# Performance work log

Measured on AMD Instinct MI355X. Metric: run time of the kernel, lower is better.

## Reference

```python
import jax, jax.numpy as jnp
import numpy as np

B, CH, H, W, D = 2, 32, 256, 512, 192


def setup_inputs() -> dict:
    key = jax.random.key(0)
    ks = jax.random.split(key, 10)
    def w(k, shape, fan_in):
        return jax.random.normal(k, shape, jnp.float32) * (1.0 / np.sqrt(fan_in))
    return {
        "x": jax.random.normal(ks[0], (B, CH, H, W), jnp.float32),
        "y": jax.random.normal(ks[1], (B, CH, H, W), jnp.float32),
        # encoder: 1x1 convs ch->64->32->1 (shared for x and y)
        "w1": w(ks[2], (64, CH), CH), "b1": w(ks[3], (64,), CH),
        "w2": w(ks[4], (32, 64), 64), "b2": w(ks[5], (32,), 64),
        "w3": w(ks[6], (1, 32), 32), "b3": w(ks[7], (1,), 32),
        # decoderl: 1x1 conv maxdisp->maxdisp (original code applies decoderl to BOTH volumes)
        "wd": w(ks[8], (D, D), D), "bd": w(ks[9], (D,), D),
    }


def _conv1x1(w, b, h):  # [O,C] x [B,C,H,W] -> [B,O,H,W]
    return jnp.einsum("oc,bchw->bohw", w, h) + b[None, :, None, None]


def _encoder(x, w1, b1, w2, b2, w3, b3):
    h = jax.nn.relu(x)
    h = jax.nn.relu(_conv1x1(w1, b1, h))
    h = jax.nn.relu(_conv1x1(w2, b2, h))
    h = jax.nn.relu(_conv1x1(w3, b3, h))
    return h[:, 0]  # squeeze channel -> [B,H,W]


def _cost_volumes(xf, yf):
    # costx[b,d,h,w] = xf[b,h,w+d] * yf[b,h,w]   (0 where w+d >= W)
    # costy[b,d,h,w] = xf[b,h,w]   * yf[b,h,w-d] (0 where w-d < 0)
    dgrid = jnp.arange(D)
    wgrid = jnp.arange(W)
    x_pad = jnp.pad(xf, ((0, 0), (0, 0), (0, D)))          # zero pad right
    xg = x_pad[:, :, wgrid[None, :] + dgrid[:, None]]       # [B,H,D,W]
    costx = (xg * yf[:, :, None, :]).transpose(0, 2, 1, 3)  # [B,D,H,W]
    y_pad = jnp.pad(yf, ((0, 0), (0, 0), (D, 0)))           # zero pad left
    yg = y_pad[:, :, wgrid[None, :] - dgrid[:, None] + D]   # [B,H,D,W]
    costy = (xf[:, :, None, :] * yg).transpose(0, 2, 1, 3)  # [B,D,H,W]
    return costx, costy


def reference(x, y, w1, b1, w2, b2, w3, b3, wd, bd):
    xf = _encoder(x, w1, b1, w2, b2, w3, b3)
    yf = _encoder(y, w1, b1, w2, b2, w3, b3)
    costx, costy = _cost_volumes(xf, yf)
    probx = jax.nn.softmax(_conv1x1(wd, bd, costx), axis=1)
    proby = jax.nn.softmax(_conv1x1(wd, bd, costy), axis=1)  # decoderl used for both, as in source
    disp_vals = jnp.arange(D, dtype=probx.dtype)
    dispx = jnp.einsum("bdhw,d->bhw", probx, disp_vals)
    dispy = jnp.einsum("bdhw,d->bhw", proby, disp_vals)
    return dispx, dispy
```

## Files before the change

kernel.cpp:

```cpp
#include <hip/hip_runtime.h>


typedef __attribute__((ext_vector_type(8)))  __bf16 bf16x8;
typedef __attribute__((ext_vector_type(4)))  float  f32x4;
typedef __attribute__((ext_vector_type(16))) float  f32x16;

#define MFMA32(a,b,c) __builtin_amdgcn_mfma_f32_32x32x16_bf16((a),(b),(c),0,0,0)
#define MFMA16(a,b,c) __builtin_amdgcn_mfma_f32_16x16x32_bf16((a),(b),(c),0,0,0)

constexpr int WW  = 512;
constexpr int HW  = 256 * 512;
constexpr int CHW = 32 * HW;
constexpr float LOG2E = 1.4426950408889634f;

constexpr size_t XFB_OFF = 0;
constexpr int    STB     = 25600;
constexpr size_t WDP_OFF = 2 * 262144 * 2;
constexpr size_t BDP_OFF = WDP_OFF + 3 * STB;

__global__ __launch_bounds__(512)
void panet_encode(const float* __restrict__ gx,  const float* __restrict__ gy,
                  const float* __restrict__ gw1, const float* __restrict__ gb1,
                  const float* __restrict__ gw2, const float* __restrict__ gb2,
                  const float* __restrict__ gw3, const float* __restrict__ gb3,
                  const float* __restrict__ gwd, const float* __restrict__ gbd,
                  char* __restrict__ ws)
{
  const int blk = blockIdx.x;
  const int tid = threadIdx.x;

  if (blk >= 1024) {
    const int pi = blk - 1024;
    unsigned short* wdp = (unsigned short*)(ws + WDP_OFF);
    for (int idx = tid; idx < 12 * 200; idx += 512) {
      const int oo = idx / 200;
      const int k  = idx - oo * 200;
      const int o  = 12 * pi + oo;
      unsigned short v = 0;
      if (k < 192) v = __builtin_bit_cast(unsigned short, (__bf16)gwd[o * 192 + k]);
      wdp[(o >> 6) * 12800 + (o & 63) * 200 + k] = v;
    }
    if (pi == 0) {
      float* bdp = (float*)(ws + BDP_OFF);
      if (tid < 192) bdp[tid] = gbd[tid] * LOG2E;
    }
    return;
  }

  const int t    = blk >> 9;
  const int bh   = blk & 511;
  const int lane = tid & 63;
  const int m    = lane & 15;
  const int g    = lane >> 4;
  const int wid  = tid >> 6;

  bf16x8 A1[4], A2[2][2];
  f32x4  bias1[4], bias2[2], w3v[2];
  #pragma unroll
  for (int Mt = 0; Mt < 4; ++Mt) {
    const float* p = gw1 + (16 * Mt + m) * 32 + 4 * g;
    const f32x4 u0 = *(const f32x4*)p;
    const f32x4 u1 = *(const f32x4*)(p + 16);
    #pragma unroll
    for (int j = 0; j < 4; ++j) { A1[Mt][j] = (__bf16)u0[j]; A1[Mt][j + 4] = (__bf16)u1[j]; }
    bias1[Mt] = *(const f32x4*)(gb1 + 16 * Mt + 4 * g);
  }
  #pragma unroll
  for (int Mt = 0; Mt < 2; ++Mt) {
    #pragma unroll
    for (int s = 0; s < 2; ++s) {
      const float* p = gw2 + (16 * Mt + m) * 64 + 32 * s + 4 * g;
      const f32x4 u0 = *(const f32x4*)p;
      const f32x4 u1 = *(const f32x4*)(p + 16);
      #pragma unroll
      for (int j = 0; j < 4; ++j) { A2[Mt][s][j] = (__bf16)u0[j]; A2[Mt][s][j + 4] = (__bf16)u1[j]; }
    }
    bias2[Mt] = *(const f32x4*)(gb2 + 16 * Mt + 4 * g);
    w3v[Mt]   = *(const f32x4*)(gw3 + 16 * Mt + 4 * g);
  }
  const float b3s = gb3[0];
  const f32x4 zf4 = {0.f, 0.f, 0.f, 0.f};
  const float* base = (t ? gy : gx) + (bh >> 8) * CHW + (bh & 255) * WW;
  unsigned short* xfb = (unsigned short*)(ws + XFB_OFF) + t * 262144 + bh * 512;

  for (int u = wid; u < 32; u += 8) {
    const int w0 = u << 4;
    const float* src = base + w0 + m;

    bf16x8 B1;
    #pragma unroll
    for (int j = 0; j < 8; ++j) {
      const int c = 16 * (j >> 2) + 4 * g + (j & 3);
      B1[j] = (__bf16)fmaxf(src[c * HW], 0.f);
    }
    f32x4 acc1[4];
    #pragma unroll
    for (int Mt = 0; Mt < 4; ++Mt) acc1[Mt] = MFMA16(A1[Mt], B1, zf4);

    bf16x8 B2[2];
    #pragma unroll
    for (int s = 0; s < 2; ++s) {
      #pragma unroll
      for (int j = 0; j < 4; ++j) {
        B2[s][j]     = (__bf16)fmaxf(acc1[2 * s][j]     + bias1[2 * s][j],     0.f);
        B2[s][j + 4] = (__bf16)fmaxf(acc1[2 * s + 1][j] + bias1[2 * s + 1][j], 0.f);
      }
    }
    f32x4 acc2[2];
    #pragma unroll
    for (int Mt = 0; Mt < 2; ++Mt)
      acc2[Mt] = MFMA16(A2[Mt][1], B2[1], MFMA16(A2[Mt][0], B2[0], zf4));

    float s3 = 0.f;
    #pragma unroll
    for (int Mt = 0; Mt < 2; ++Mt)
      #pragma unroll
      for (int r = 0; r < 4; ++r)
        s3 += w3v[Mt][r] * fmaxf(acc2[Mt][r] + bias2[Mt][r], 0.f);
    s3 += __shfl_xor(s3, 16);
    s3 += __shfl_xor(s3, 32);
    const float val = fmaxf(s3 + b3s, 0.f);

    if (lane < 16)
      xfb[w0 + m] = __builtin_bit_cast(unsigned short, (__bf16)val);
  }
}

constexpr int CPS    = 1424;
constexpr int K2_HK  = 76800;
constexpr int K2_BD  = K2_HK + 8 * CPS;
constexpr int K2_LDS = K2_BD + 768;

__global__ __launch_bounds__(512)
void panet_corr(const char* __restrict__ ws, float* __restrict__ gout)
{
  __shared__ __align__(16) char lds[K2_LDS];
  const int blk  = blockIdx.x;
  const int dir  = blk >> 9;
  const int bh   = blk & 511;
  const int tid  = threadIdx.x;
  const int lane = tid & 63;
  const int l31  = lane & 31;
  const int h    = lane >> 5;
  const int wid  = tid >> 6;

  const unsigned short* xfbu = (const unsigned short*)(ws + XFB_OFF);
  const unsigned short* hs = xfbu + (dir ? 262144 : 0) + bh * 512;
  const unsigned short* ss = xfbu + (dir ? 0 : 262144) + bh * 512;

  {
    const f32x4* src = (const f32x4*)(ws + WDP_OFF);
    f32x4* dst = (f32x4*)lds;
    #pragma unroll 5
    for (int i = tid; i < 4800; i += 512) dst[i] = src[i];
    if (tid < 192)
      ((float*)(lds + K2_BD))[tid] = ((const float*)(ws + BDP_OFF))[tid];
  }
  for (int e = tid; e < 712; e += 512) {
    #pragma unroll
    for (int c = 0; c < 8; ++c) {
      const int j = e + c;
      unsigned short v = 0;
      if (j <= 511) v = hs[dir ? (511 - j) : j];
      ((unsigned short*)(lds + K2_HK + c * CPS))[e] = v;
    }
  }
  __syncthreads();

  const char* bptr[2]; float sc[2];
  #pragma unroll
  for (int ct = 0; ct < 2; ++ct) {
    const int col = wid * 64 + ct * 32 + l31;
    const int I0  = dir ? (511 - col) : col;
    const int cc  = I0 & 7;
    bptr[ct] = lds + K2_HK + cc * CPS + 2 * (I0 - cc) + 16 * h;
    sc[ct]  = LOG2E * __builtin_bit_cast(float, (unsigned)ss[col] << 16);
  }

  float stS0 = 0.f, stS1 = 0.f, stW0 = 0.f, stW1 = 0.f;

  for (int s = 0; s < 3; ++s) {
    const char* abase = lds + (64 * s + l31) * 400 + 16 * h;
    f32x16 a00 = {0}, a01 = {0}, a10 = {0}, a11 = {0};
    #pragma unroll 4
    for (int ks = 0; ks < 12; ++ks) {
      const bf16x8 af0 = *(const bf16x8*)(abase + 32 * ks);
      const bf16x8 af1 = *(const bf16x8*)(abase + 12800 + 32 * ks);
      const bf16x8 bf0 = *(const bf16x8*)(bptr[0] + 32 * ks);
      const bf16x8 bf1 = *(const bf16x8*)(bptr[1] + 32 * ks);
      a00 = MFMA32(af0, bf0, a00);
      a01 = MFMA32(af0, bf1, a01);
      a10 = MFMA32(af1, bf0, a10);
      a11 = MFMA32(af1, bf1, a11);
    }

    f32x4 bdr0[4], bdr1[4];
    #pragma unroll
    for (int q = 0; q < 4; ++q) {
      bdr0[q] = *(const f32x4*)(lds + K2_BD + (64 * s + 8 * q + 4 * h) * 4);
      bdr1[q] = *(const f32x4*)(lds + K2_BD + (64 * s + 8 * q + 4 * h + 32) * 4);
    }
    const float obase = (float)(64 * s + 4 * h);

    #pragma unroll
    for (int ct = 0; ct < 2; ++ct) {
      float ls0 = 0.f, ls1 = 0.f, lw0 = 0.f, lw1 = 0.f;
      #pragma unroll
      for (int q = 0; q < 4; ++q) {
        #pragma unroll
        for (int r = 0; r < 4; ++r) {
          const int i = 4 * q + r;
          const float L0 = fmaf(sc[ct], (ct ? a01 : a00)[i], bdr0[q][r]);
          const float L1 = fmaf(sc[ct], (ct ? a11 : a10)[i], bdr1[q][r]);
          const float p0 = __builtin_amdgcn_exp2f(L0);
          const float p1 = __builtin_amdgcn_exp2f(L1);
          const float c  = (float)(r + 8 * q);
          ls0 += p0;  ls1 += p1;
          lw0 = fmaf(c, p0, lw0);
          lw1 = fmaf(c + 32.f, p1, lw1);
        }
      }
      const float ls = ls0 + ls1;
      const float lw = fmaf(obase, ls, lw0 + lw1);
      if (ct == 0) { stS0 += ls; stW0 += lw; }
      else         { stS1 += ls; stW1 += lw; }
    }
  }

  float* outp = gout + dir * 262144 + bh * 512;
  #pragma unroll
  for (int ct = 0; ct < 2; ++ct) {
    float sr = ct ? stS1 : stS0;
    float wr = ct ? stW1 : stW0;
    sr += __shfl_xor(sr, 32);
    wr += __shfl_xor(wr, 32);
    if (lane < 32) outp[wid * 64 + ct * 32 + l31] = wr / sr;
  }
}

extern "C" void kernel_launch(void* const* d_in, const int* in_sizes, int n_in,
                              void* d_out, int out_size, void* d_ws, size_t ws_size,
                              hipStream_t stream) {
  const float* x  = (const float*)d_in[0];
  const float* y  = (const float*)d_in[1];
  const float* w1 = (const float*)d_in[2];
  const float* b1 = (const float*)d_in[3];
  const float* w2 = (const float*)d_in[4];
  const float* b2 = (const float*)d_in[5];
  const float* w3 = (const float*)d_in[6];
  const float* b3 = (const float*)d_in[7];
  const float* wd = (const float*)d_in[8];
  const float* bd = (const float*)d_in[9];
  char* ws = (char*)d_ws;

  panet_encode<<<1040, 512, 0, stream>>>(x, y, w1, b1, w2, b2, w3, b3, wd, bd, ws);
  panet_corr<<<1024, 512, 0, stream>>>(ws, (float*)d_out);
}
```

Baseline: 81.36 us.

## Halve corr block size and give each wave four column tiles

The correlation kernel now runs 256 threads per block, and each wave computes 128 output columns (four 32-wide tiles) instead of 64. Each A-fragment load from LDS is reused across four MFMAs instead of two, which cuts LDS traffic per MFMA and halves the per-block weight-staging cost per wave. In exchange each wave holds twice as many accumulators (8 f32x16 tiles), which raises register pressure and may lower occupancy. With fewer waves per block, each wave also does more of the LDS fill.

```diff
diff --git a/kernel.cpp b/kernel.cpp
--- a/kernel.cpp
+++ b/kernel.cpp
@@ -131,7 +131,7 @@
 constexpr int K2_BD  = K2_HK + 8 * CPS;
 constexpr int K2_LDS = K2_BD + 768;
 
-__global__ __launch_bounds__(512)
+__global__ __launch_bounds__(256)
 void panet_corr(const char* __restrict__ ws, float* __restrict__ gout)
 {
   __shared__ __align__(16) char lds[K2_LDS];
@@ -151,12 +151,12 @@
   {
     const f32x4* src = (const f32x4*)(ws + WDP_OFF);
     f32x4* dst = (f32x4*)lds;
-    #pragma unroll 5
-    for (int i = tid; i < 4800; i += 512) dst[i] = src[i];
+    #pragma unroll 4
+    for (int i = tid; i < 4800; i += 256) dst[i] = src[i];
     if (tid < 192)
       ((float*)(lds + K2_BD))[tid] = ((const float*)(ws + BDP_OFF))[tid];
   }
-  for (int e = tid; e < 712; e += 512) {
+  for (int e = tid; e < 712; e += 256) {
     #pragma unroll
     for (int c = 0; c < 8; ++c) {
       const int j = e + c;
@@ -167,51 +167,51 @@
   }
   __syncthreads();
 
-  const char* bptr[2]; float sc[2];
-  #pragma unroll
-  for (int ct = 0; ct < 2; ++ct) {
-    const int col = wid * 64 + ct * 32 + l31;
+  int boff[4]; float sc[4];
+  #pragma unroll
+  for (int ct = 0; ct < 4; ++ct) {
+    const int col = wid * 128 + ct * 32 + l31;
     const int I0  = dir ? (511 - col) : col;
     const int cc  = I0 & 7;
-    bptr[ct] = lds + K2_HK + cc * CPS + 2 * (I0 - cc) + 16 * h;
+    boff[ct] = K2_HK + cc * CPS + 2 * (I0 - cc) + 16 * h;
     sc[ct]  = LOG2E * __builtin_bit_cast(float, (unsigned)ss[col] << 16);
   }
 
-  float stS0 = 0.f, stS1 = 0.f, stW0 = 0.f, stW1 = 0.f;
+  float stS[4] = {0.f, 0.f, 0.f, 0.f};
+  float stW[4] = {0.f, 0.f, 0.f, 0.f};
 
   for (int s = 0; s < 3; ++s) {
     const char* abase = lds + (64 * s + l31) * 400 + 16 * h;
-    f32x16 a00 = {0}, a01 = {0}, a10 = {0}, a11 = {0};
-    #pragma unroll 4
+    f32x16 a0[4] = {{0}, {0}, {0}, {0}};
+    f32x16 a1[4] = {{0}, {0}, {0}, {0}};
+    #pragma unroll 2
     for (int ks = 0; ks < 12; ++ks) {
       const bf16x8 af0 = *(const bf16x8*)(abase + 32 * ks);
       const bf16x8 af1 = *(const bf16x8*)(abase + 12800 + 32 * ks);
-      const bf16x8 bf0 = *(const bf16x8*)(bptr[0] + 32 * ks);
-      const bf16x8 bf1 = *(const bf16x8*)(bptr[1] + 32 * ks);
-      a00 = MFMA32(af0, bf0, a00);
-      a01 = MFMA32(af0, bf1, a01);
-      a10 = MFMA32(af1, bf0, a10);
-      a11 = MFMA32(af1, bf1, a11);
-    }
-
-    f32x4 bdr0[4], bdr1[4];
-    #pragma unroll
-    for (int q = 0; q < 4; ++q) {
-      bdr0[q] = *(const f32x4*)(lds + K2_BD + (64 * s + 8 * q + 4 * h) * 4);
-      bdr1[q] = *(const f32x4*)(lds + K2_BD + (64 * s + 8 * q + 4 * h + 32) * 4);
-    }
+      bf16x8 bf[4];
+      #pragma unroll
+      for (int ct = 0; ct < 4; ++ct)
+        bf[ct] = *(const bf16x8*)(lds + boff[ct] + 32 * ks);
+      #pragma unroll
+      for (int ct = 0; ct < 4; ++ct) {
+        a0[ct] = MFMA32(af0, bf[ct], a0[ct]);
+        a1[ct] = MFMA32(af1, bf[ct], a1[ct]);
+      }
+    }
+
     const float obase = (float)(64 * s + 4 * h);
-
-    #pragma unroll
-    for (int ct = 0; ct < 2; ++ct) {
+    #pragma unroll
+    for (int ct = 0; ct < 4; ++ct) {
       float ls0 = 0.f, ls1 = 0.f, lw0 = 0.f, lw1 = 0.f;
       #pragma unroll
       for (int q = 0; q < 4; ++q) {
+        const f32x4 bd0 = *(const f32x4*)(lds + K2_BD + (64 * s + 8 * q + 4 * h) * 4);
+        const f32x4 bd1 = *(const f32x4*)(lds + K2_BD + (64 * s + 8 * q + 4 * h + 32) * 4);
         #pragma unroll
         for (int r = 0; r < 4; ++r) {
           const int i = 4 * q + r;
-          const float L0 = fmaf(sc[ct], (ct ? a01 : a00)[i], bdr0[q][r]);
-          const float L1 = fmaf(sc[ct], (ct ? a11 : a10)[i], bdr1[q][r]);
+          const float L0 = fmaf(sc[ct], a0[ct][i], bd0[r]);
+          const float L1 = fmaf(sc[ct], a1[ct][i], bd1[r]);
           const float p0 = __builtin_amdgcn_exp2f(L0);
           const float p1 = __builtin_amdgcn_exp2f(L1);
           const float c  = (float)(r + 8 * q);
@@ -222,19 +222,19 @@
       }
       const float ls = ls0 + ls1;
       const float lw = fmaf(obase, ls, lw0 + lw1);
-      if (ct == 0) { stS0 += ls; stW0 += lw; }
-      else         { stS1 += ls; stW1 += lw; }
+      stS[ct] += ls;
+      stW[ct] += lw;
     }
   }
 
   float* outp = gout + dir * 262144 + bh * 512;
   #pragma unroll
-  for (int ct = 0; ct < 2; ++ct) {
-    float sr = ct ? stS1 : stS0;
-    float wr = ct ? stW1 : stW0;
+  for (int ct = 0; ct < 4; ++ct) {
+    float sr = stS[ct];
+    float wr = stW[ct];
     sr += __shfl_xor(sr, 32);
     wr += __shfl_xor(wr, 32);
-    if (lane < 32) outp[wid * 64 + ct * 32 + l31] = wr / sr;
+    if (lane < 32) outp[wid * 128 + ct * 32 + l31] = wr / sr;
   }
 }
 
@@ -254,5 +254,5 @@
   char* ws = (char*)d_ws;
 
   panet_encode<<<1040, 512, 0, stream>>>(x, y, w1, b1, w2, b2, w3, b3, wd, bd, ws);
-  panet_corr<<<1024, 512, 0, stream>>>(ws, (float*)d_out);
+  panet_corr<<<1024, 256, 0, stream>>>(ws, (float*)d_out);
 }
```

New measurement: 85.78 us. 5.4% more time.
